# Optimization experiments

Measured on AMD Instinct MI355X. Metric: run time of the kernel, lower is better.

## Reference

```python
import jax, jax.numpy as jnp
import numpy as np

B, E_DIM, N_EXP, EXP_SZ, N_TASKS, TOPK = 16384, 512, 16, 512, 2, 3
D_IN = 2 * E_DIM      # 1024
D_HID = 4 * E_DIM     # 2048
EPS = 1e-5


def _ln(x, g, b):
    mu = jnp.mean(x, axis=-1, keepdims=True)
    var = jnp.var(x, axis=-1, keepdims=True)
    return (x - mu) * jax.lax.rsqrt(var + EPS) * g + b


def setup_inputs() -> dict:
    key = jax.random.key(0)
    ks = jax.random.split(key, 24)
    def w(k, shape, fan_in):
        return jax.random.normal(k, shape, jnp.float32) * (1.0 / np.sqrt(fan_in))
    return {
        "emb_paper": jax.random.normal(ks[0], (B, E_DIM), jnp.float32),
        "emb_reviewer": jax.random.normal(ks[1], (B, E_DIM), jnp.float32),
        # interaction encoder
        "enc_W1": w(ks[2], (D_IN, D_HID), D_IN), "enc_b1": jnp.zeros((D_HID,), jnp.float32),
        "ln1_g": jnp.ones((D_HID,), jnp.float32), "ln1_b": jnp.zeros((D_HID,), jnp.float32),
        "enc_W2": w(ks[3], (D_HID, D_IN), D_HID), "enc_b2": jnp.zeros((D_IN,), jnp.float32),
        "ln2_g": jnp.ones((D_IN,), jnp.float32), "ln2_b": jnp.zeros((D_IN,), jnp.float32),
        # per-task gates (stacked over task axis)
        "gW1": w(ks[4], (N_TASKS, D_IN, 128), D_IN), "gb1": jnp.zeros((N_TASKS, 128), jnp.float32),
        "gW2": w(ks[5], (N_TASKS, 128, N_EXP), 128), "gb2": jnp.zeros((N_TASKS, N_EXP), jnp.float32),
        # stacked experts
        "We1": w(ks[6], (N_EXP, D_IN, EXP_SZ), D_IN), "be1": jnp.zeros((N_EXP, EXP_SZ), jnp.float32),
        "We2": w(ks[7], (N_EXP, EXP_SZ, EXP_SZ), EXP_SZ), "be2": jnp.zeros((N_EXP, EXP_SZ), jnp.float32),
        # per-task towers
        "tW1": w(ks[8], (N_TASKS, EXP_SZ, 256), EXP_SZ), "tb1": jnp.zeros((N_TASKS, 256), jnp.float32),
        "tW2": w(ks[9], (N_TASKS, 256, 128), 256), "tb2": jnp.zeros((N_TASKS, 128), jnp.float32),
        "tW3": w(ks[10], (N_TASKS, 128, 1), 128), "tb3": jnp.zeros((N_TASKS, 1), jnp.float32),
        "task_idx": 0,
    }


def reference(emb_paper, emb_reviewer, enc_W1, enc_b1, ln1_g, ln1_b, enc_W2, enc_b2,
              ln2_g, ln2_b, gW1, gb1, gW2, gb2, We1, be1, We2, be2,
              tW1, tb1, tW2, tb2, tW3, tb3, task_idx):
    # interaction encoder (eval mode: dropout is identity)
    x = jnp.concatenate([emb_paper, emb_reviewer], axis=-1)          # [B, 2E]
    h = jax.nn.relu(_ln(x @ enc_W1 + enc_b1, ln1_g, ln1_b))          # [B, 4E]
    feat = _ln(h @ enc_W2 + enc_b2, ln2_g, ln2_b)                    # [B, 2E]

    # task gate -> top-k sparse softmax gates (no router noise in eval)
    g = jax.nn.relu(feat @ gW1[task_idx] + gb1[task_idx])
    logits = g @ gW2[task_idx] + gb2[task_idx]                       # [B, E]
    top_s, top_i = jax.lax.top_k(logits, TOPK)                       # [B, k]
    gates = jnp.zeros_like(logits).at[jnp.arange(logits.shape[0])[:, None], top_i].set(
        jax.nn.softmax(top_s, axis=-1))

    # dense expert stack (faithful to original: all experts computed)
    e1 = jax.nn.relu(jnp.einsum('bi,eio->beo', feat, We1) + be1[None])   # [B, E, S]
    eo = jnp.einsum('beo,eoh->beh', e1, We2) + be2[None]                 # [B, E, S]
    mix = jnp.einsum('be,beh->bh', gates, eo)                            # [B, S]

    # task tower
    t = jax.nn.relu(mix @ tW1[task_idx] + tb1[task_idx])
    t = jax.nn.relu(t @ tW2[task_idx] + tb2[task_idx])
    out = jax.nn.sigmoid(t @ tW3[task_idx] + tb3[task_idx]).squeeze(-1)  # [B]
    return out, task_idx, gates
```

## Files before the change

kernel.cpp:

```cpp
#include <hip/hip_runtime.h>

typedef __attribute__((ext_vector_type(8))) _Float16 f16x8;
typedef __attribute__((ext_vector_type(4))) float f32x4;

#define DEVINL __device__ __forceinline__

constexpr int BATCH = 16384;
constexpr int DIN   = 1024;
constexpr int DHID  = 2048;
constexpr int NEXP  = 16;
constexpr int EXPSZ = 512;
constexpr int NPAIR = BATCH * 3;

DEVINL unsigned short f2h(float v) {
  _Float16 h = (_Float16)v;
  return __builtin_bit_cast(unsigned short, h);
}
DEVINL float h2f(unsigned short u) {
  return (float)__builtin_bit_cast(_Float16, u);
}

DEVINL void gl2lds(const unsigned short* src, char* ldst) {
  __builtin_amdgcn_global_load_lds((const __attribute__((address_space(1))) void*)src,
                                   (__attribute__((address_space(3))) void*)ldst, 16, 0, 0);
}

template<int SPLIT, int ASTAGE, int AMODE, int EPI, int BK, int NYT, int TASK>
__global__ __launch_bounds__(256, SPLIT ? 2 : 3)
void mgemm_k(const unsigned short* __restrict__ A0p,
             const unsigned short* __restrict__ A1p,
             const float* __restrict__ Af0, const float* __restrict__ Af1,
             const unsigned short* __restrict__ B0p,
             const unsigned short* __restrict__ B1p,
             const float* __restrict__ biasb,
             float* __restrict__ Cf, unsigned short* __restrict__ Cb0,
             unsigned short* __restrict__ Cb1,
             const int* __restrict__ pairRow, const float* __restrict__ pairW,
             const int* __restrict__ counts, const int* __restrict__ offs,
             const int* __restrict__ taskPtr,
             int M, int N, int K)
{
  constexpr int KG = BK / 8;
  constexpr int UNITS = 128 * KG;
  constexpr int ISS = UNITS / 256;
  constexpr int NKK = BK / 32;
  constexpr int NARR = SPLIT ? 4 : 2;
  constexpr bool EXPERT = (AMODE == 1 || AMODE == 2);
  __shared__ char smem[NARR * UNITS * 16];
  char* sA0 = smem;
  char* sA1 = smem + UNITS * 16;
  char* sB0 = smem + (SPLIT ? 2 : 1) * UNITS * 16;
  char* sB1 = smem + 3 * UNITS * 16;

  int Mloc = M, rowBase = 0;
  const unsigned short* b0 = B0p;
  const unsigned short* b1 = B1p;
  const float* bias = biasb;
  if (EXPERT) {
    const int e = blockIdx.z;
    Mloc = counts[e];
    rowBase = offs[e];
    const size_t eo = (size_t)e * (size_t)K * N;
    b0 = B0p + eo;
    if (SPLIT) b1 = B1p + eo;
    bias = biasb + (size_t)e * N;
  }
  if (TASK) bias = biasb + (size_t)(*taskPtr) * N;

  const int xcd = (int)blockIdx.x & 7;
  const int j   = (int)blockIdx.x >> 3;
  const int tile0 = (xcd + 8 * (j / NYT)) * 128;
  const int col0  = (j % NYT) * 128;
  if (tile0 >= Mloc) return;

  const int tid = threadIdx.x;
  const int lane = tid & 63;
  const int wr = ((tid >> 6) >> 1) * 64;
  const int wc = ((tid >> 6) & 1) * 64;
  const int l15 = lane & 15;
  const int lg = lane >> 4;

  const int srow = tid & 127;
  size_t aoff = 0;
  const float* aF = nullptr;
  const float* aP = nullptr;
  const float* aR = nullptr;
  if (ASTAGE) {
    if (AMODE == 3) {
      aP = Af0 + (size_t)(tile0 + srow) * 512;
      aR = Af1 + (size_t)(tile0 + srow) * 512;
    } else {
      aF = Af0 + (size_t)(tile0 + srow) * K;
    }
  } else if (AMODE == 0) {
    aoff = (size_t)(tile0 + srow) * K;
  } else if (AMODE == 1) {
    int p = rowBase + tile0 + srow; p = p < NPAIR - 1 ? p : NPAIR - 1;
    aoff = (size_t)pairRow[p] * K;
  } else {
    int p = rowBase + tile0 + srow; p = p < NPAIR - 1 ? p : NPAIR - 1;
    aoff = (size_t)p * K;
  }
  const size_t boff = (size_t)(col0 + srow) * K;

  f32x4 acc[4][4];
  f32x4 acc2[4][4];
  #pragma unroll
  for (int m = 0; m < 4; ++m)
    #pragma unroll
    for (int n = 0; n < 4; ++n) {
      acc[m][n] = f32x4{0.f, 0.f, 0.f, 0.f};
      if (SPLIT) acc2[m][n] = f32x4{0.f, 0.f, 0.f, 0.f};
    }

  for (int kt = 0; kt < K; kt += BK) {
    if (ASTAGE) {
      #pragma unroll
      for (int it = 0; it < ISS; ++it) {
        const int u = it * 256 + tid;
        const int ko = kt + (u >> 7) * 8;
        const float* s;
        if (AMODE == 3) s = (ko < 512) ? (aP + ko) : (aR + (ko - 512));
        else            s = aF + ko;
        const float4 x0 = *(const float4*)s;
        const float4 x1 = *(const float4*)(s + 4);
        const float vv[8] = {x0.x, x0.y, x0.z, x0.w, x1.x, x1.y, x1.z, x1.w};
        f16x8 q0, q1;
        #pragma unroll
        for (int jq = 0; jq < 8; ++jq) {
          const _Float16 c0 = (_Float16)vv[jq];
          q0[jq] = c0;
          if (SPLIT) q1[jq] = (_Float16)((vv[jq] - (float)c0) * 2048.f);
        }
        *(f16x8*)(sA0 + (size_t)u * 16) = q0;
        if (SPLIT) *(f16x8*)(sA1 + (size_t)u * 16) = q1;
      }
    }
    #pragma unroll
    for (int it = 0; it < ISS; ++it) {
      const int uo = (it * 256 + (tid & 192)) * 16;
      const int ko = kt + (it * 2 + (tid >> 7)) * 8;
      if (!ASTAGE) {
        gl2lds(A0p + aoff + ko, sA0 + uo);
        if (SPLIT) gl2lds(A1p + aoff + ko, sA1 + uo);
      }
      gl2lds(b0 + boff + ko, sB0 + uo);
      if (SPLIT) gl2lds(b1 + boff + ko, sB1 + uo);
    }
    __syncthreads();
    #pragma unroll
    for (int kk = 0; kk < NKK; ++kk) {
      const int g = kk * 4 + lg;
      f16x8 b0f[4], b1f[4];
      #pragma unroll
      for (int n = 0; n < 4; ++n) {
        const size_t off = (size_t)(g * 128 + wc + n * 16 + l15) * 16;
        b0f[n] = *(const f16x8*)(sB0 + off);
        if (SPLIT) b1f[n] = *(const f16x8*)(sB1 + off);
      }
      #pragma unroll
      for (int m = 0; m < 4; ++m) {
        const size_t ao = (size_t)(g * 128 + wr + m * 16 + l15) * 16;
        const f16x8 a0 = *(const f16x8*)(sA0 + ao);
        f16x8 a1;
        if (SPLIT) a1 = *(const f16x8*)(sA1 + ao);
        #pragma unroll
        for (int n = 0; n < 4; ++n) {
          if (SPLIT) {
            acc2[m][n] = __builtin_amdgcn_mfma_f32_16x16x32_f16(a1, b0f[n], acc2[m][n], 0, 0, 0);
            acc2[m][n] = __builtin_amdgcn_mfma_f32_16x16x32_f16(a0, b1f[n], acc2[m][n], 0, 0, 0);
          }
          acc[m][n] = __builtin_amdgcn_mfma_f32_16x16x32_f16(a0, b0f[n], acc[m][n], 0, 0, 0);
        }
      }
    }
    __syncthreads();
  }

  #pragma unroll
  for (int n = 0; n < 4; ++n) {
    const int cn = col0 + wc + n * 16 + l15;
    const float bv = bias[cn];
    #pragma unroll
    for (int m = 0; m < 4; ++m) {
      const int r0 = wr + m * 16 + ((lane >> 4) << 2);
      #pragma unroll
      for (int jj = 0; jj < 4; ++jj) {
        const int rm = tile0 + r0 + jj;
        if (EXPERT && rm >= Mloc) continue;
        float v = acc[m][n][jj];
        if (SPLIT) v += acc2[m][n][jj] * (1.f / 2048.f);
        v += bv;
        const size_t ci = (size_t)(EXPERT ? (rowBase + rm) : rm) * N + cn;
        if (EPI == 0) {
          const unsigned short h0 = f2h(v);
          Cb0[ci] = h0;
          Cb1[ci] = f2h((v - h2f(h0)) * 2048.f);
        } else if (EPI == 1) {
          Cb0[ci] = f2h(fmaxf(v, 0.f));
        } else if (EPI == 2) {
          Cb0[ci] = f2h(v * pairW[rowBase + rm]);
        } else if (EPI == 3) {
          Cf[ci] = v;
        } else {
          Cf[ci] = fmaxf(v, 0.f);
        }
      }
    }
  }
}

template<int LEV, int TASK>
__global__ __launch_bounds__(256)
void transp_k(const float* __restrict__ src, unsigned short* __restrict__ d0,
              unsigned short* __restrict__ d1, const int* __restrict__ taskPtr,
              int R, int C)
{
  __shared__ float tle[32][33];
  size_t bb = (size_t)blockIdx.z * R * C;
  if (TASK) bb = (size_t)(*taskPtr) * R * C;
  const int r0 = blockIdx.x * 32, c0 = blockIdx.y * 32;
  const int x = threadIdx.x & 31, y = threadIdx.x >> 5;
  #pragma unroll
  for (int i = 0; i < 32; i += 8)
    tle[y + i][x] = src[bb + (size_t)(r0 + y + i) * C + (c0 + x)];
  __syncthreads();
  const size_t db = TASK ? 0 : (size_t)blockIdx.z * R * C;
  #pragma unroll
  for (int i = 0; i < 32; i += 8) {
    const float v = tle[x][y + i];
    const size_t di = db + (size_t)(c0 + y + i) * R + (r0 + x);
    const unsigned short h0 = f2h(v);
    d0[di] = h0;
    if (LEV > 1) d1[di] = f2h((v - h2f(h0)) * 2048.f);
  }
}

template<int COLS, bool RELU>
__global__ __launch_bounds__(256)
void ln_k(float* __restrict__ x, const float* __restrict__ g, const float* __restrict__ b)
{
  constexpr int PER = COLS / 256;
  const size_t row = blockIdx.x;
  float* xr = x + row * COLS;
  float v[PER];
  float s = 0.f, s2 = 0.f;
  #pragma unroll
  for (int i = 0; i < PER; ++i) {
    v[i] = xr[threadIdx.x + i * 256];
    s += v[i];
    s2 += v[i] * v[i];
  }
  #pragma unroll
  for (int o = 1; o < 64; o <<= 1) { s += __shfl_xor(s, o); s2 += __shfl_xor(s2, o); }
  __shared__ float ss[4], ss2[4];
  const int w = threadIdx.x >> 6;
  if ((threadIdx.x & 63) == 0) { ss[w] = s; ss2[w] = s2; }
  __syncthreads();
  s  = ss[0] + ss[1] + ss[2] + ss[3];
  s2 = ss2[0] + ss2[1] + ss2[2] + ss2[3];
  const float mu = s * (1.f / COLS);
  const float var = s2 * (1.f / COLS) - mu * mu;
  const float rs = rsqrtf(var + 1e-5f);
  #pragma unroll
  for (int i = 0; i < PER; ++i) {
    const int c = threadIdx.x + i * 256;
    float y = (v[i] - mu) * rs * g[c] + b[c];
    if (RELU) y = fmaxf(y, 0.f);
    xr[c] = y;
  }
}

template<int COLS, bool RELU>
__global__ __launch_bounds__(256)
void ln_pair_k(unsigned short* __restrict__ h0, unsigned short* __restrict__ h1,
               const float* __restrict__ g, const float* __restrict__ b)
{
  constexpr int PER = COLS / 256;
  const size_t row = blockIdx.x;
  unsigned short* r0 = h0 + row * COLS;
  unsigned short* r1 = h1 + row * COLS;
  const int c0 = threadIdx.x * PER;
  float v[PER];
  float s = 0.f, s2 = 0.f;
  #pragma unroll
  for (int i = 0; i < PER; i += 4) {
    const ushort4 a = *(const ushort4*)(r0 + c0 + i);
    const ushort4 c = *(const ushort4*)(r1 + c0 + i);
    v[i+0] = h2f(a.x) + h2f(c.x) * (1.f/2048.f);
    v[i+1] = h2f(a.y) + h2f(c.y) * (1.f/2048.f);
    v[i+2] = h2f(a.z) + h2f(c.z) * (1.f/2048.f);
    v[i+3] = h2f(a.w) + h2f(c.w) * (1.f/2048.f);
  }
  #pragma unroll
  for (int i = 0; i < PER; ++i) { s += v[i]; s2 += v[i] * v[i]; }
  #pragma unroll
  for (int o = 1; o < 64; o <<= 1) { s += __shfl_xor(s, o); s2 += __shfl_xor(s2, o); }
  __shared__ float ss[4], ss2[4];
  const int w = threadIdx.x >> 6;
  if ((threadIdx.x & 63) == 0) { ss[w] = s; ss2[w] = s2; }
  __syncthreads();
  s  = ss[0] + ss[1] + ss[2] + ss[3];
  s2 = ss2[0] + ss2[1] + ss2[2] + ss2[3];
  const float mu = s * (1.f / COLS);
  const float var = s2 * (1.f / COLS) - mu * mu;
  const float rs = rsqrtf(var + 1e-5f);
  #pragma unroll
  for (int i = 0; i < PER; i += 4) {
    ushort4 a4, c4v;
    unsigned short* ap = (unsigned short*)&a4;
    unsigned short* cp = (unsigned short*)&c4v;
    #pragma unroll
    for (int jq = 0; jq < 4; ++jq) {
      const int c = c0 + i + jq;
      float y = (v[i+jq] - mu) * rs * g[c] + b[c];
      if (RELU) y = fmaxf(y, 0.f);
      const unsigned short hh = f2h(y);
      ap[jq] = hh;
      cp[jq] = f2h((y - h2f(hh)) * 2048.f);
    }
    *(ushort4*)(r0 + c0 + i) = a4;
    *(ushort4*)(r1 + c0 + i) = c4v;
  }
}

__global__ __launch_bounds__(256)
void gate_topk_k(const float* __restrict__ g, const float* __restrict__ gW2,
                 const float* __restrict__ gb2, const int* __restrict__ taskPtr,
                 float* __restrict__ gatesOut, int* __restrict__ topkIdx,
                 float* __restrict__ topkW)
{
  const int t = *taskPtr;
  const float* W = gW2 + (size_t)t * 128 * 16;
  const float* bias = gb2 + (size_t)t * 16;
  const int lane = threadIdx.x & 63;
  const int row = blockIdx.x * 4 + (threadIdx.x >> 6);
  const float* gr = g + (size_t)row * 128;
  const int e = lane & 15;
  const int q = lane >> 4;
  float s = 0.f;
  for (int j = q * 32; j < q * 32 + 32; ++j) s = fmaf(gr[j], W[j * 16 + e], s);
  s += __shfl_xor(s, 16);
  s += __shfl_xor(s, 32);
  s += bias[e];
  float logits[16];
  #pragma unroll
  for (int i = 0; i < 16; ++i) logits[i] = __shfl(s, i);
  int i0 = 0; float v0 = logits[0];
  #pragma unroll
  for (int i = 1; i < 16; ++i) if (logits[i] > v0) { v0 = logits[i]; i0 = i; }
  int i1 = -1; float v1 = -3.4e38f;
  #pragma unroll
  for (int i = 0; i < 16; ++i) if (i != i0 && logits[i] > v1) { v1 = logits[i]; i1 = i; }
  int i2 = -1; float v2 = -3.4e38f;
  #pragma unroll
  for (int i = 0; i < 16; ++i) if (i != i0 && i != i1 && logits[i] > v2) { v2 = logits[i]; i2 = i; }
  const float ex1 = expf(v1 - v0);
  const float ex2 = expf(v2 - v0);
  const float inv = 1.f / (1.f + ex1 + ex2);
  const float p0 = inv, p1 = ex1 * inv, p2 = ex2 * inv;
  if (lane < 16) {
    const float gv = (lane == i0) ? p0 : (lane == i1) ? p1 : (lane == i2) ? p2 : 0.f;
    gatesOut[(size_t)row * 16 + lane] = gv;
  }
  if (lane == 0) {
    topkIdx[row * 3 + 0] = i0; topkIdx[row * 3 + 1] = i1; topkIdx[row * 3 + 2] = i2;
    topkW [row * 3 + 0] = p0; topkW [row * 3 + 1] = p1; topkW [row * 3 + 2] = p2;
  }
}

__global__ __launch_bounds__(256)
void hist_k(const int* __restrict__ topkIdx, int* __restrict__ chunkCnt)
{
  __shared__ int lc[NEXP];
  if (threadIdx.x < NEXP) lc[threadIdx.x] = 0;
  __syncthreads();
  const int row = blockIdx.x * 256 + threadIdx.x;
  #pragma unroll
  for (int k = 0; k < 3; ++k) atomicAdd(&lc[topkIdx[row * 3 + k]], 1);
  __syncthreads();
  if (threadIdx.x < NEXP) chunkCnt[blockIdx.x * NEXP + threadIdx.x] = lc[threadIdx.x];
}

__global__ void scanB_k(const int* __restrict__ chunkCnt, int* __restrict__ counts,
                        int* __restrict__ offs, int* __restrict__ chunkBase)
{
  if (threadIdx.x == 0) {
    int tot[NEXP];
    for (int e = 0; e < NEXP; ++e) tot[e] = 0;
    for (int c = 0; c < 64; ++c)
      for (int e = 0; e < NEXP; ++e) tot[e] += chunkCnt[c * NEXP + e];
    int a = 0;
    for (int e = 0; e < NEXP; ++e) { offs[e] = a; counts[e] = tot[e]; a += tot[e]; }
    for (int e = 0; e < NEXP; ++e) {
      int b = offs[e];
      for (int c = 0; c < 64; ++c) { chunkBase[c * NEXP + e] = b; b += chunkCnt[c * NEXP + e]; }
    }
  }
}

__global__ __launch_bounds__(256)
void fill2_k(const int* __restrict__ topkIdx, const float* __restrict__ topkW,
             const int* __restrict__ chunkBase, int* __restrict__ pairRow,
             float* __restrict__ pairW, int* __restrict__ rowPos)
{
  __shared__ int lc[NEXP];
  if (threadIdx.x < NEXP) lc[threadIdx.x] = 0;
  __syncthreads();
  const int row = blockIdx.x * 256 + threadIdx.x;
  #pragma unroll
  for (int k = 0; k < 3; ++k) {
    const int e = topkIdx[row * 3 + k];
    const int lofs = atomicAdd(&lc[e], 1);
    const int pos = chunkBase[blockIdx.x * NEXP + e] + lofs;
    pairRow[pos] = row;
    pairW[pos] = topkW[row * 3 + k];
    rowPos[row * 3 + k] = pos;
  }
}

__global__ __launch_bounds__(256)
void mixreduce_k(const unsigned short* __restrict__ eo, const int* __restrict__ rowPos,
                 unsigned short* __restrict__ mix16)
{
  const size_t row = blockIdx.x;
  const size_t p0 = rowPos[row * 3 + 0];
  const size_t p1 = rowPos[row * 3 + 1];
  const size_t p2 = rowPos[row * 3 + 2];
  for (int c = threadIdx.x; c < EXPSZ; c += 256) {
    mix16[row * EXPSZ + c] = f2h(h2f(eo[p0 * EXPSZ + c]) + h2f(eo[p1 * EXPSZ + c])
                               + h2f(eo[p2 * EXPSZ + c]));
  }
}

__global__ __launch_bounds__(256)
void tower3_k(const unsigned short* __restrict__ t2, const float* __restrict__ tW3,
              const float* __restrict__ tb3, const int* __restrict__ taskPtr,
              float* __restrict__ out)
{
  const int t = *taskPtr;
  const float* w = tW3 + (size_t)t * 128;
  const float bias = tb3[t];
  const int lane = threadIdx.x & 63;
  const int row = blockIdx.x * 4 + (threadIdx.x >> 6);
  const unsigned short* x = t2 + (size_t)row * 128;
  float s = fmaf(h2f(x[lane]), w[lane], h2f(x[lane + 64]) * w[lane + 64]);
  #pragma unroll
  for (int o = 1; o < 64; o <<= 1) s += __shfl_xor(s, o);
  if (lane == 0) out[row] = 1.f / (1.f + expf(-(s + bias)));
  if (blockIdx.x == 0 && threadIdx.x == 0) out[BATCH] = (float)t;
}

extern "C" void kernel_launch(void* const* d_in, const int* in_sizes, int n_in,
                              void* d_out, int out_size, void* d_ws, size_t ws_size,
                              hipStream_t stream)
{
  (void)in_sizes; (void)n_in; (void)out_size; (void)ws_size;
  const float* embP  = (const float*)d_in[0];
  const float* embR  = (const float*)d_in[1];
  const float* encW1 = (const float*)d_in[2];
  const float* encB1 = (const float*)d_in[3];
  const float* ln1g  = (const float*)d_in[4];
  const float* ln1b  = (const float*)d_in[5];
  const float* encW2 = (const float*)d_in[6];
  const float* encB2 = (const float*)d_in[7];
  const float* ln2g  = (const float*)d_in[8];
  const float* ln2b  = (const float*)d_in[9];
  const float* gW1   = (const float*)d_in[10];
  const float* gb1   = (const float*)d_in[11];
  const float* gW2   = (const float*)d_in[12];
  const float* gb2   = (const float*)d_in[13];
  const float* We1   = (const float*)d_in[14];
  const float* be1   = (const float*)d_in[15];
  const float* We2   = (const float*)d_in[16];
  const float* be2   = (const float*)d_in[17];
  const float* tW1   = (const float*)d_in[18];
  const float* tb1   = (const float*)d_in[19];
  const float* tW2   = (const float*)d_in[20];
  const float* tb2   = (const float*)d_in[21];
  const float* tW3   = (const float*)d_in[22];
  const float* tb3   = (const float*)d_in[23];
  const int* taskPtr = (const int*)d_in[24];

  float* out = (float*)d_out;
  char* ws = (char*)d_ws;
  const size_t MB = 1ull << 20;

  unsigned short* feat0 = (unsigned short*)(ws);
  unsigned short* feat1 = (unsigned short*)(ws + 32 * MB);
  unsigned short* mix16 = (unsigned short*)(ws + 32 * MB);
  unsigned short* t1f16 = (unsigned short*)(ws + 48 * MB);
  unsigned short* t2f16 = (unsigned short*)(ws + 56 * MB);
  float* h = (float*)(ws + 64 * MB);
  unsigned short* We1t0 = (unsigned short*)(ws + 64 * MB);
  unsigned short* We2t0 = (unsigned short*)(ws + 80 * MB);
  unsigned short* e1b   = (unsigned short*)(ws + 88 * MB);
  unsigned short* eob   = (unsigned short*)(ws + 136 * MB);
  unsigned short* W1t0  = (unsigned short*)(ws + 192 * MB);
  unsigned short* W1t1  = (unsigned short*)(ws + 196 * MB);
  unsigned short* W2t0  = (unsigned short*)(ws + 200 * MB);
  unsigned short* W2t1  = (unsigned short*)(ws + 204 * MB);
  unsigned short* gW1t0 = (unsigned short*)(ws + 200 * MB);
  unsigned short* gW1t1 = (unsigned short*)(ws + 204 * MB);
  float* gbuf = (float*)(ws + 192 * MB);
  unsigned short* tW1t = (unsigned short*)(ws + 192 * MB);
  unsigned short* tW2t = (unsigned short*)(ws + 193 * MB);
  char* small = ws + 208 * MB;
  int*   counts    = (int*)  (small);
  int*   offs      = (int*)  (small + 1024);
  int*   chunkCnt  = (int*)  (small + 2048);
  int*   chunkBase = (int*)  (small + 2048 + 4096);
  int*   topkIdx   = (int*)  (small + 16384);
  float* topkW     = (float*)(small + 16384 + 196608);
  int*   pairRow   = (int*)  (small + 16384 + 2 * 196608);
  float* pairW     = (float*)(small + 16384 + 3 * 196608);
  int*   rowPos    = (int*)  (small + 16384 + 4 * 196608);

  const dim3 blk(256, 1, 1);

  transp_k<2,0><<<dim3(DIN/32, DHID/32, 1), blk, 0, stream>>>(encW1, W1t0, W1t1, nullptr, DIN, DHID);
  mgemm_k<1,1,3,3,32,DHID/128,0><<<dim3((BATCH/128)*(DHID/128), 1, 1), blk, 0, stream>>>(
      nullptr, nullptr, embP, embR, W1t0, W1t1, encB1, h, nullptr, nullptr,
      nullptr, nullptr, nullptr, nullptr, nullptr, BATCH, DHID, DIN);
  ln_k<DHID, true><<<dim3(BATCH, 1, 1), blk, 0, stream>>>(h, ln1g, ln1b);

  transp_k<2,0><<<dim3(DHID/32, DIN/32, 1), blk, 0, stream>>>(encW2, W2t0, W2t1, nullptr, DHID, DIN);
  mgemm_k<1,1,0,0,32,DIN/128,0><<<dim3((BATCH/128)*(DIN/128), 1, 1), blk, 0, stream>>>(
      nullptr, nullptr, h, nullptr, W2t0, W2t1, encB2, nullptr, feat0, feat1,
      nullptr, nullptr, nullptr, nullptr, nullptr, BATCH, DIN, DHID);
  ln_pair_k<DIN, false><<<dim3(BATCH, 1, 1), blk, 0, stream>>>(feat0, feat1, ln2g, ln2b);

  transp_k<2,1><<<dim3(DIN/32, 128/32, 1), blk, 0, stream>>>(gW1, gW1t0, gW1t1, taskPtr, DIN, 128);
  mgemm_k<1,0,0,4,64,1,1><<<dim3(BATCH/128, 1, 1), blk, 0, stream>>>(
      feat0, feat1, nullptr, nullptr, gW1t0, gW1t1, gb1, gbuf, nullptr, nullptr,
      nullptr, nullptr, nullptr, nullptr, taskPtr, BATCH, 128, DIN);
  gate_topk_k<<<dim3(BATCH/4, 1, 1), blk, 0, stream>>>(
      gbuf, gW2, gb2, taskPtr, out + BATCH + 1, topkIdx, topkW);
  hist_k<<<dim3(BATCH/256, 1, 1), blk, 0, stream>>>(topkIdx, chunkCnt);
  scanB_k<<<dim3(1, 1, 1), dim3(64, 1, 1), 0, stream>>>(chunkCnt, counts, offs, chunkBase);
  fill2_k<<<dim3(BATCH/256, 1, 1), blk, 0, stream>>>(topkIdx, topkW, chunkBase,
                                                     pairRow, pairW, rowPos);

  transp_k<1,0><<<dim3(DIN/32, EXPSZ/32, NEXP), blk, 0, stream>>>(We1, We1t0, nullptr, nullptr, DIN, EXPSZ);
  transp_k<1,0><<<dim3(EXPSZ/32, EXPSZ/32, NEXP), blk, 0, stream>>>(We2, We2t0, nullptr, nullptr, EXPSZ, EXPSZ);

  mgemm_k<0,0,1,1,64,EXPSZ/128,0><<<dim3((BATCH/128)*(EXPSZ/128), 1, NEXP), blk, 0, stream>>>(
      feat0, nullptr, nullptr, nullptr, We1t0, nullptr, be1, nullptr, e1b, nullptr,
      pairRow, nullptr, counts, offs, nullptr, NPAIR, EXPSZ, DIN);
  mgemm_k<0,0,2,2,64,EXPSZ/128,0><<<dim3((BATCH/128)*(EXPSZ/128), 1, NEXP), blk, 0, stream>>>(
      e1b, nullptr, nullptr, nullptr, We2t0, nullptr, be2, nullptr, eob, nullptr,
      nullptr, pairW, counts, offs, nullptr, NPAIR, EXPSZ, EXPSZ);
  mixreduce_k<<<dim3(BATCH, 1, 1), blk, 0, stream>>>(eob, rowPos, mix16);

  transp_k<1,1><<<dim3(EXPSZ/32, 256/32, 1), blk, 0, stream>>>(tW1, tW1t, nullptr, taskPtr, EXPSZ, 256);
  transp_k<1,1><<<dim3(256/32, 128/32, 1), blk, 0, stream>>>(tW2, tW2t, nullptr, taskPtr, 256, 128);
  mgemm_k<0,0,0,1,64,2,1><<<dim3((BATCH/128)*2, 1, 1), blk, 0, stream>>>(
      mix16, nullptr, nullptr, nullptr, tW1t, nullptr, tb1, nullptr, t1f16, nullptr,
      nullptr, nullptr, nullptr, nullptr, taskPtr, BATCH, 256, EXPSZ);
  mgemm_k<0,0,0,1,64,1,1><<<dim3(BATCH/128, 1, 1), blk, 0, stream>>>(
      t1f16, nullptr, nullptr, nullptr, tW2t, nullptr, tb2, nullptr, t2f16, nullptr,
      nullptr, nullptr, nullptr, nullptr, taskPtr, BATCH, 128, 256);
  tower3_k<<<dim3(BATCH/4, 1, 1), blk, 0, stream>>>(t2f16, tW3, tb3, taskPtr, out);
}
```

Before: 1.110 ms.

## Double-buffer LDS tiles in the MFMA GEMM to overlap loads with compute

The GEMM kernel now allocates two LDS stage buffers. It issues the global-to-LDS loads (or register prefetch plus f16 conversion for staged-A paths) for the next K tile while MFMAs run on the current one, which removes one barrier per iteration and hides global load latency. To keep LDS usage bounded, the BK=64 launches are cut to BK=32, so each stage is smaller but there are more iterations. The cost is doubled shared memory per block, which may reduce occupancy, plus extra registers held for the prefetch.

After: 1.055 ms. -5.0%, faster.

```diff
diff --git a/kernel.cpp b/kernel.cpp
--- a/kernel.cpp
+++ b/kernel.cpp
@@ -45,12 +45,9 @@
   constexpr int ISS = UNITS / 256;
   constexpr int NKK = BK / 32;
   constexpr int NARR = SPLIT ? 4 : 2;
+  constexpr size_t BUFSZ = (size_t)NARR * UNITS * 16;
   constexpr bool EXPERT = (AMODE == 1 || AMODE == 2);
-  __shared__ char smem[NARR * UNITS * 16];
-  char* sA0 = smem;
-  char* sA1 = smem + UNITS * 16;
-  char* sB0 = smem + (SPLIT ? 2 : 1) * UNITS * 16;
-  char* sB1 = smem + 3 * UNITS * 16;
+  __shared__ char smem[2 * NARR * UNITS * 16];
 
   int Mloc = M, rowBase = 0;
   const unsigned short* b0 = B0p;
@@ -113,12 +110,16 @@
       if (SPLIT) acc2[m][n] = f32x4{0.f, 0.f, 0.f, 0.f};
     }
 
-  for (int kt = 0; kt < K; kt += BK) {
+  {
+    char* dA0 = smem;
+    char* dA1 = smem + UNITS * 16;
+    char* dB0 = smem + (SPLIT ? 2 : 1) * UNITS * 16;
+    char* dB1 = smem + 3 * (size_t)UNITS * 16;
     if (ASTAGE) {
       #pragma unroll
       for (int it = 0; it < ISS; ++it) {
         const int u = it * 256 + tid;
-        const int ko = kt + (u >> 7) * 8;
+        const int ko = (u >> 7) * 8;
         const float* s;
         if (AMODE == 3) s = (ko < 512) ? (aP + ko) : (aR + (ko - 512));
         else            s = aF + ko;
@@ -132,49 +133,118 @@
           q0[jq] = c0;
           if (SPLIT) q1[jq] = (_Float16)((vv[jq] - (float)c0) * 2048.f);
         }
-        *(f16x8*)(sA0 + (size_t)u * 16) = q0;
-        if (SPLIT) *(f16x8*)(sA1 + (size_t)u * 16) = q1;
+        *(f16x8*)(dA0 + (size_t)u * 16) = q0;
+        if (SPLIT) *(f16x8*)(dA1 + (size_t)u * 16) = q1;
       }
     }
     #pragma unroll
     for (int it = 0; it < ISS; ++it) {
       const int uo = (it * 256 + (tid & 192)) * 16;
-      const int ko = kt + (it * 2 + (tid >> 7)) * 8;
+      const int ko = (it * 2 + (tid >> 7)) * 8;
       if (!ASTAGE) {
-        gl2lds(A0p + aoff + ko, sA0 + uo);
-        if (SPLIT) gl2lds(A1p + aoff + ko, sA1 + uo);
+        gl2lds(A0p + aoff + ko, dA0 + uo);
+        if (SPLIT) gl2lds(A1p + aoff + ko, dA1 + uo);
       }
-      gl2lds(b0 + boff + ko, sB0 + uo);
-      if (SPLIT) gl2lds(b1 + boff + ko, sB1 + uo);
-    }
-    __syncthreads();
-    #pragma unroll
-    for (int kk = 0; kk < NKK; ++kk) {
-      const int g = kk * 4 + lg;
-      f16x8 b0f[4], b1f[4];
-      #pragma unroll
-      for (int n = 0; n < 4; ++n) {
-        const size_t off = (size_t)(g * 128 + wc + n * 16 + l15) * 16;
-        b0f[n] = *(const f16x8*)(sB0 + off);
-        if (SPLIT) b1f[n] = *(const f16x8*)(sB1 + off);
+      gl2lds(b0 + boff + ko, dB0 + uo);
+      if (SPLIT) gl2lds(b1 + boff + ko, dB1 + uo);
+    }
+  }
+  __syncthreads();
+
+  const int NT = K / BK;
+  int cur = 0;
+  for (int t = 0; t < NT; ++t) {
+    const int nxt = cur ^ 1;
+    const int ktn = (t + 1) * BK;
+    const bool hav = (t + 1 < NT);
+    char* nA0 = smem + (size_t)nxt * BUFSZ;
+    char* nA1 = nA0 + UNITS * 16;
+    char* nB0 = nA0 + (SPLIT ? 2 : 1) * UNITS * 16;
+    char* nB1 = nA0 + 3 * (size_t)UNITS * 16;
+
+    float4 pf0[ISS], pf1[ISS];
+    if (hav) {
+      if (ASTAGE) {
+        #pragma unroll
+        for (int it = 0; it < ISS; ++it) {
+          const int u = it * 256 + tid;
+          const int ko = ktn + (u >> 7) * 8;
+          const float* s;
+          if (AMODE == 3) s = (ko < 512) ? (aP + ko) : (aR + (ko - 512));
+          else            s = aF + ko;
+          pf0[it] = *(const float4*)s;
+          pf1[it] = *(const float4*)(s + 4);
+        }
+      } else {
+        #pragma unroll
+        for (int it = 0; it < ISS; ++it) {
+          const int uo = (it * 256 + (tid & 192)) * 16;
+          const int ko = ktn + (it * 2 + (tid >> 7)) * 8;
+          gl2lds(A0p + aoff + ko, nA0 + uo);
+          if (SPLIT) gl2lds(A1p + aoff + ko, nA1 + uo);
+        }
       }
       #pragma unroll
-      for (int m = 0; m < 4; ++m) {
-        const size_t ao = (size_t)(g * 128 + wr + m * 16 + l15) * 16;
-        const f16x8 a0 = *(const f16x8*)(sA0 + ao);
-        f16x8 a1;
-        if (SPLIT) a1 = *(const f16x8*)(sA1 + ao);
+      for (int it = 0; it < ISS; ++it) {
+        const int uo = (it * 256 + (tid & 192)) * 16;
+        const int ko = ktn + (it * 2 + (tid >> 7)) * 8;
+        gl2lds(b0 + boff + ko, nB0 + uo);
+        if (SPLIT) gl2lds(b1 + boff + ko, nB1 + uo);
+      }
+    }
+
+    {
+      char* cA0 = smem + (size_t)cur * BUFSZ;
+      char* cA1 = cA0 + UNITS * 16;
+      char* cB0 = cA0 + (SPLIT ? 2 : 1) * UNITS * 16;
+      char* cB1 = cA0 + 3 * (size_t)UNITS * 16;
+      #pragma unroll
+      for (int kk = 0; kk < NKK; ++kk) {
+        const int g = kk * 4 + lg;
+        f16x8 b0f[4], b1f[4];
         #pragma unroll
         for (int n = 0; n < 4; ++n) {
-          if (SPLIT) {
-            acc2[m][n] = __builtin_amdgcn_mfma_f32_16x16x32_f16(a1, b0f[n], acc2[m][n], 0, 0, 0);
-            acc2[m][n] = __builtin_amdgcn_mfma_f32_16x16x32_f16(a0, b1f[n], acc2[m][n], 0, 0, 0);
+          const size_t off = (size_t)(g * 128 + wc + n * 16 + l15) * 16;
+          b0f[n] = *(const f16x8*)(cB0 + off);
+          if (SPLIT) b1f[n] = *(const f16x8*)(cB1 + off);
+        }
+        #pragma unroll
+        for (int m = 0; m < 4; ++m) {
+          const size_t ao = (size_t)(g * 128 + wr + m * 16 + l15) * 16;
+          const f16x8 a0 = *(const f16x8*)(cA0 + ao);
+          f16x8 a1;
+          if (SPLIT) a1 = *(const f16x8*)(cA1 + ao);
+          #pragma unroll
+          for (int n = 0; n < 4; ++n) {
+            if (SPLIT) {
+              acc2[m][n] = __builtin_amdgcn_mfma_f32_16x16x32_f16(a1, b0f[n], acc2[m][n], 0, 0, 0);
+              acc2[m][n] = __builtin_amdgcn_mfma_f32_16x16x32_f16(a0, b1f[n], acc2[m][n], 0, 0, 0);
+            }
+            acc[m][n] = __builtin_amdgcn_mfma_f32_16x16x32_f16(a0, b0f[n], acc[m][n], 0, 0, 0);
           }
-          acc[m][n] = __builtin_amdgcn_mfma_f32_16x16x32_f16(a0, b0f[n], acc[m][n], 0, 0, 0);
         }
       }
     }
+
+    if (hav && ASTAGE) {
+      #pragma unroll
+      for (int it = 0; it < ISS; ++it) {
+        const int u = it * 256 + tid;
+        const float vv[8] = {pf0[it].x, pf0[it].y, pf0[it].z, pf0[it].w,
+                             pf1[it].x, pf1[it].y, pf1[it].z, pf1[it].w};
+        f16x8 q0, q1;
+        #pragma unroll
+        for (int jq = 0; jq < 8; ++jq) {
+          const _Float16 c0 = (_Float16)vv[jq];
+          q0[jq] = c0;
+          if (SPLIT) q1[jq] = (_Float16)((vv[jq] - (float)c0) * 2048.f);
+        }
+        *(f16x8*)(nA0 + (size_t)u * 16) = q0;
+        if (SPLIT) *(f16x8*)(nA1 + (size_t)u * 16) = q1;
+      }
+    }
     __syncthreads();
+    cur = nxt;
   }
 
   #pragma unroll
@@ -531,7 +601,7 @@
   ln_pair_k<DIN, false><<<dim3(BATCH, 1, 1), blk, 0, stream>>>(feat0, feat1, ln2g, ln2b);
 
   transp_k<2,1><<<dim3(DIN/32, 128/32, 1), blk, 0, stream>>>(gW1, gW1t0, gW1t1, taskPtr, DIN, 128);
-  mgemm_k<1,0,0,4,64,1,1><<<dim3(BATCH/128, 1, 1), blk, 0, stream>>>(
+  mgemm_k<1,0,0,4,32,1,1><<<dim3(BATCH/128, 1, 1), blk, 0, stream>>>(
       feat0, feat1, nullptr, nullptr, gW1t0, gW1t1, gb1, gbuf, nullptr, nullptr,
       nullptr, nullptr, nullptr, nullptr, taskPtr, BATCH, 128, DIN);
   gate_topk_k<<<dim3(BATCH/4, 1, 1), blk, 0, stream>>>(
@@ -544,20 +614,20 @@
   transp_k<1,0><<<dim3(DIN/32, EXPSZ/32, NEXP), blk, 0, stream>>>(We1, We1t0, nullptr, nullptr, DIN, EXPSZ);
   transp_k<1,0><<<dim3(EXPSZ/32, EXPSZ/32, NEXP), blk, 0, stream>>>(We2, We2t0, nullptr, nullptr, EXPSZ, EXPSZ);
 
-  mgemm_k<0,0,1,1,64,EXPSZ/128,0><<<dim3((BATCH/128)*(EXPSZ/128), 1, NEXP), blk, 0, stream>>>(
+  mgemm_k<0,0,1,1,32,EXPSZ/128,0><<<dim3((BATCH/128)*(EXPSZ/128), 1, NEXP), blk, 0, stream>>>(
       feat0, nullptr, nullptr, nullptr, We1t0, nullptr, be1, nullptr, e1b, nullptr,
       pairRow, nullptr, counts, offs, nullptr, NPAIR, EXPSZ, DIN);
-  mgemm_k<0,0,2,2,64,EXPSZ/128,0><<<dim3((BATCH/128)*(EXPSZ/128), 1, NEXP), blk, 0, stream>>>(
+  mgemm_k<0,0,2,2,32,EXPSZ/128,0><<<dim3((BATCH/128)*(EXPSZ/128), 1, NEXP), blk, 0, stream>>>(
       e1b, nullptr, nullptr, nullptr, We2t0, nullptr, be2, nullptr, eob, nullptr,
       nullptr, pairW, counts, offs, nullptr, NPAIR, EXPSZ, EXPSZ);
   mixreduce_k<<<dim3(BATCH, 1, 1), blk, 0, stream>>>(eob, rowPos, mix16);
 
   transp_k<1,1><<<dim3(EXPSZ/32, 256/32, 1), blk, 0, stream>>>(tW1, tW1t, nullptr, taskPtr, EXPSZ, 256);
   transp_k<1,1><<<dim3(256/32, 128/32, 1), blk, 0, stream>>>(tW2, tW2t, nullptr, taskPtr, 256, 128);
-  mgemm_k<0,0,0,1,64,2,1><<<dim3((BATCH/128)*2, 1, 1), blk, 0, stream>>>(
+  mgemm_k<0,0,0,1,32,2,1><<<dim3((BATCH/128)*2, 1, 1), blk, 0, stream>>>(
       mix16, nullptr, nullptr, nullptr, tW1t, nullptr, tb1, nullptr, t1f16, nullptr,
       nullptr, nullptr, nullptr, nullptr, taskPtr, BATCH, 256, EXPSZ);
-  mgemm_k<0,0,0,1,64,1,1><<<dim3(BATCH/128, 1, 1), blk, 0, stream>>>(
+  mgemm_k<0,0,0,1,32,1,1><<<dim3(BATCH/128, 1, 1), blk, 0, stream>>>(
       t1f16, nullptr, nullptr, nullptr, tW2t, nullptr, tb2, nullptr, t2f16, nullptr,
       nullptr, nullptr, nullptr, nullptr, taskPtr, BATCH, 128, 256);
   tower3_k<<<dim3(BATCH/4, 1, 1), blk, 0, stream>>>(t2f16, tW3, tb3, taskPtr, out);
```
